# Kernel tuning notes

Hardware: AMD Instinct MI355X
Metric: run time of the kernel (lower is better)

## Reference

```python
import jax, jax.numpy as jnp
import numpy as np

B, T, N, CIN = 64, 24, 256, 1  # batch, n_his, n stations, in channels
F1, F2, OUTC = 64, 128, 1      # blocks [[64,64],[64,128]], output channels
K = 3                          # conv kernel size


def conv2d_same(x, w):  # x [B,H,W,C], w [K,K,C,O]
    return jax.lax.conv_general_dilated(x, w, (1, 1), 'SAME',
                                        dimension_numbers=('NHWC', 'HWIO', 'NHWC'))


def conv1d_same(x, w):  # x [B,N,C], w [K,C,O]
    return jax.lax.conv_general_dilated(x, w, (1,), 'SAME',
                                        dimension_numbers=('NWC', 'WIO', 'NWC'))


def hard_sigmoid(x):  # keras ConvLSTM default recurrent_activation
    return jnp.clip(x * 0.2 + 0.5, 0.0, 1.0)


def l2_normalize_23(x):  # tf.nn.l2_normalize over axes [2,3]
    sq = jnp.sum(x * x, axis=(2, 3), keepdims=True)
    return x * jax.lax.rsqrt(jnp.maximum(sq, 1e-12))


def convlstm1d(x_seq, kx, kh, b, return_sequences):
    # x_seq [B,T,N,C]; kx [K,C,4F]; kh [K,F,4F]; b [4F]
    Bs, Ts, Ns, Cs = x_seq.shape
    F = kh.shape[1]
    # input convolutions are time-independent: do them all at once
    xg = conv1d_same(x_seq.reshape(Bs * Ts, Ns, Cs), kx).reshape(Bs, Ts, Ns, 4 * F) + b
    xg = jnp.moveaxis(xg, 1, 0)  # [T,B,N,4F]
    h0 = jnp.zeros((Bs, Ns, F), x_seq.dtype)
    c0 = jnp.zeros((Bs, Ns, F), x_seq.dtype)

    def step(carry, xt):
        h, c = carry
        g = xt + conv1d_same(h, kh)                 # [B,N,4F]
        gi, gf, gc, go = jnp.split(g, 4, axis=-1)
        i = hard_sigmoid(gi)
        f = hard_sigmoid(gf)
        o = hard_sigmoid(go)
        c = f * c + i * jnp.tanh(gc)
        h = o * jnp.tanh(c)
        return (h, c), (h if return_sequences else jnp.zeros((), x_seq.dtype))

    (hT, _), hs = jax.lax.scan(step, (h0, c0), xg)
    if return_sequences:
        return jnp.moveaxis(hs, 0, 1)  # [B,T,N,F]
    return hT                          # [B,N,F]


def setup_inputs() -> dict:
    key = jax.random.key(0)
    ks = jax.random.split(key, 14)
    s = 0.1
    return {
        'x': jax.random.normal(ks[0], (B, T, N, CIN), jnp.float32),
        'conv1_w': jax.random.normal(ks[1], (K, K, CIN, F1), jnp.float32) * s,
        'conv1_b': jnp.zeros((F1,), jnp.float32),
        'conv2_w': jax.random.normal(ks[2], (K, K, F1, F1), jnp.float32) * s,
        'conv2_b': jnp.zeros((F1,), jnp.float32),
        'kx1': jax.random.normal(ks[3], (K, F1, 4 * F1), jnp.float32) * s,
        'kh1': jax.random.normal(ks[4], (K, F1, 4 * F1), jnp.float32) * s,
        'b1': jnp.zeros((4 * F1,), jnp.float32),
        'kx2': jax.random.normal(ks[5], (K, F1, 4 * F2), jnp.float32) * s,
        'kh2': jax.random.normal(ks[6], (K, F2, 4 * F2), jnp.float32) * s,
        'b2': jnp.zeros((4 * F2,), jnp.float32),
        'fc_w': jax.random.normal(ks[7], (F2, OUTC), jnp.float32) * s,
        'fc_b': jnp.zeros((OUTC,), jnp.float32),
    }


def reference(x, conv1_w, conv1_b, conv2_w, conv2_b, kx1, kh1, b1,
              kx2, kh2, b2, fc_w, fc_b):
    # spatial conv stack (Conv2D 3x3 same, linear activation)
    h = conv2d_same(x, conv1_w) + conv1_b
    h = conv2d_same(h, conv2_w) + conv2_b
    # dropout = identity at inference; norm == 'L2'
    h = l2_normalize_23(h)
    # stacked ConvLSTM1D: return_sequences=True then False
    h = convlstm1d(h, kx1, kh1, b1, True)    # [B,T,N,F1]
    h = convlstm1d(h, kx2, kh2, b2, False)   # [B,N,F2]
    h = h[:, None]                            # reshape (-1, 1, N, F2)
    h = l2_normalize_23(h)
    # FullyConLayer: 1x1 FC over channels -> outc
    y = jnp.einsum('bunc,co->buno', h, fc_w) + fc_b
    return y.reshape(-1, 1, N, OUTC)
```

## Files before the change

### kernel.cpp

```cpp
#include <hip/hip_runtime.h>
#include <hip/hip_bf16.h>

using bf16 = __hip_bfloat16;
typedef unsigned short u16;
typedef unsigned int u32;
typedef __attribute__((ext_vector_type(8))) short short8;
typedef __attribute__((ext_vector_type(4))) float floatx4;

#define DEVI __device__ __forceinline__

constexpr int B = 64, T = 24, N = 256, F1 = 64, F2 = 128;

DEVI float b2f(bf16 v) { return __bfloat162float(v); }
DEVI float b2fu(u16 u) { return __uint_as_float(((u32)u) << 16); }
DEVI u16 f2b(float f) {
    u32 u = __float_as_uint(f);
    u32 r = (u + 0x7FFF + ((u >> 16) & 1)) >> 16;
    return (u16)r;
}
DEVI float hsig(float x) { x = x * 0.2f + 0.5f; return fminf(fmaxf(x, 0.f), 1.f); }

#if __has_builtin(__builtin_amdgcn_global_load_lds)
#define ASYNC16(gsrc, ldst)                                                            \
    __builtin_amdgcn_global_load_lds((const __attribute__((address_space(1))) u32*)(gsrc), \
                                     (__attribute__((address_space(3))) u32*)(ldst), 16, 0, 0)
#define HAVE_ASYNC 1
#else
#define HAVE_ASYNC 0
#endif

DEVI float read_in(const void* p, long i, int isbf) {
    return isbf ? b2f(((const bf16*)p)[i]) : ((const float*)p)[i];
}

__global__ void init_flag(int* flag) { *flag = 1; }
__global__ void detect_scan(const u16* __restrict__ xu, int* __restrict__ flag) {
    int i0 = blockIdx.x * 2048 + threadIdx.x;
    int hit = 0;
    for (int i = i0; i < (blockIdx.x + 1) * 2048; i += 256)
        if (((xu[i] >> 7) & 0xFF) == 0xFF) hit = 1;
    if (hit) *flag = 0;
}

struct CvtDesc { const void* src; float* dst; int n; };
struct CvtPack { CvtDesc d[8]; };
__global__ void cvt_pack(CvtPack p, const int* __restrict__ flag) {
    CvtDesc c = p.d[blockIdx.x];
    int isbf = *flag;
    for (int i = threadIdx.x; i < c.n; i += 256)
        c.dst[i] = c.src ? read_in(c.src, i, isbf) : 0.f;
}

__global__ void repack_w(const void* __restrict__ kxr, const void* __restrict__ khr,
                         u16* __restrict__ Wt, int CIN, int F, const int* __restrict__ flag) {
    int NG = 4 * F, CH = CIN + F, K = 3 * CH;
    int idx = blockIdx.x * 256 + threadIdx.x;
    if (idx >= NG * K) return;
    int g = idx / K, k = idx - g * K;
    int kn = k / CH, c = k - kn * CH;
    int isbf = *flag;
    float v = (c < CIN) ? read_in(kxr, (long)(kn * CIN + c) * NG + g, isbf)
                        : read_in(khr, (long)(kn * F + (c - CIN)) * NG + g, isbf);
    Wt[(long)g * K + k] = f2b(v);
}

__global__ void repack_w2(const void* __restrict__ w2r, u16* __restrict__ w2b,
                          const int* __restrict__ flag) {
    int idx = blockIdx.x * 256 + threadIdx.x;
    if (idx >= 64 * 576) return;
    int f = idx / 576, k = idx - f * 576;
    int kt = k / 192, rem = k - kt * 192, kn = rem >> 6, c = rem & 63;
    float v = read_in(w2r, (long)((kt * 3 + kn) * 64 + c) * 64 + f, *flag);
    w2b[(long)f * 576 + k] = f2b(v);
}

__global__ __launch_bounds__(256)
void conv1_all(const void* __restrict__ xraw, const float* __restrict__ w1c,
               const float* __restrict__ b1v, u16* __restrict__ c1all,
               const int* __restrict__ flag) {
    __shared__ float sxw[3 * 260];
    int s = blockIdx.x, b = blockIdx.y, tid = threadIdx.x;
    int tt = s - 1;
    u16* dst = c1all + ((long)s * B + b) * N * 64;
    if (tt < 0 || tt >= T) {
        for (int i = tid; i < N * 64 / 4; i += 256) *(uint2*)&dst[i * 4] = uint2{0, 0};
        return;
    }
    int isbf = *flag;
    for (int i = tid; i < 3 * 258; i += 256) {
        int r = i / 258, cc = i - r * 258;
        int ttt = tt - 1 + r, nn = cc - 1;
        float v = 0.f;
        if (ttt >= 0 && ttt < T && nn >= 0 && nn < N)
            v = read_in(xraw, (long)(b * T + ttt) * N + nn, isbf);
        sxw[r * 260 + cc] = v;
    }
    __syncthreads();
    int c = tid & 63, ngq = tid >> 6;
    float w[9];
#pragma unroll
    for (int j = 0; j < 9; j++) w[j] = w1c[j * 64 + c];
    float bias = b1v[c];
    for (int j = 0; j < 64; j++) {
        int n = ngq * 64 + j;
        float v = bias;
#pragma unroll
        for (int dt = 0; dt < 3; dt++)
#pragma unroll
            for (int dn = 0; dn < 3; dn++)
                v += sxw[dt * 260 + n + dn] * w[dt * 3 + dn];
        dst[n * 64 + c] = f2b(v);
    }
}

__global__ __launch_bounds__(256)
void conv_mfma(const u16* __restrict__ c1all, const u16* __restrict__ w2b,
               const float* __restrict__ b2v, u16* __restrict__ xs24,
               float* __restrict__ ssq) {
    constexpr int CP1 = 72;
    __shared__ __align__(16) u16 win1[3 * 66 * CP1];
    __shared__ __align__(16) u16 bch[2 * 2048];
    __shared__ float red[256];

    int tid = threadIdx.x;
    int bb = blockIdx.y, n0 = blockIdx.x * 64, t = blockIdx.z;
    int w = tid >> 6, l15 = tid & 15, q = (tid >> 4) & 3;

    for (int i = tid; i < 3 * 66 * 8; i += 256) {
        int u = i & 7, rr = i >> 3;
        int kt = rr / 66, r1 = rr - kt * 66;
        int nn = n0 - 1 + r1;
        uint4 v{0, 0, 0, 0};
        if (nn >= 0 && nn < N)
            v = *(const uint4*)&c1all[((((long)(t + kt)) * B + bb) * N + nn) * 64 + u * 8];
        *(uint4*)&win1[(kt * 66 + r1) * CP1 + u * 8] = v;
    }

    auto stage = [&](int kk, int bufi) {
        int g = tid >> 2, u = tid & 3;
        int k = kk * 32 + ((u ^ (g & 3)) << 3);
#if HAVE_ASYNC
        ASYNC16(w2b + (long)g * 576 + k, &bch[bufi * 2048 + tid * 8]);
#else
        uint4 v = *(const uint4*)(w2b + (long)g * 576 + k);
        *(uint4*)&bch[bufi * 2048 + tid * 8] = v;
#endif
    };
    stage(0, 0);
    __syncthreads();

    floatx4 acc[4] = {};
    for (int kk = 0; kk < 18; ++kk) {
        int cur = kk & 1;
        if (kk + 1 < 18) stage(kk + 1, 1 - cur);
        int kbase = kk * 32;
        int kt = kbase / 192, rem = kbase - kt * 192, kn = rem >> 6, c0 = rem & 63;
        int gcol = w * 16 + l15;
        short8 bf = *(const short8*)&bch[cur * 2048 + gcol * 32 + ((q ^ (gcol & 3)) << 3)];
#pragma unroll
        for (int mi = 0; mi < 4; mi++) {
            short8 af = *(const short8*)&win1[(kt * 66 + mi * 16 + l15 + kn) * CP1 + c0 + q * 8];
            acc[mi] = __builtin_amdgcn_mfma_f32_16x16x32_bf16(af, bf, acc[mi], 0, 0, 0);
        }
        __syncthreads();
    }

    u16* xslice = xs24 + (long)t * B * N * 64;
    int f = w * 16 + l15;
    float bias2 = b2v[f];
    float lsum = 0.f;
#pragma unroll
    for (int mi = 0; mi < 4; mi++)
#pragma unroll
        for (int r = 0; r < 4; r++) {
            int n = n0 + mi * 16 + q * 4 + r;
            float v = acc[mi][r] + bias2;
            lsum += v * v;
            xslice[((long)bb * N + n) * 64 + f] = f2b(v);
        }
    red[tid] = lsum; __syncthreads();
    for (int k = 128; k > 0; k >>= 1) {
        if (tid < k) red[tid] += red[tid + k];
        __syncthreads();
    }
    if (tid == 0) atomicAdd(&ssq[bb * T + t], red[0]);
}

template<int CIN, int F, int FL>
__global__ __launch_bounds__(512, 4)
void lstm_mfma(const u16* __restrict__ xin, const u16* __restrict__ hprev,
               u16* __restrict__ hnext, float* __restrict__ cst,
               const u16* __restrict__ Wt, const float* __restrict__ bias,
               const float* __restrict__ ssqp, int t) {
    constexpr int CH = CIN + F;
    constexpr int CHP = CH + 8;
    constexpr int K = 3 * CH;
    constexpr int NK = K / 32;
    constexpr int NGL = 4 * FL;
    constexpr int NGP = NGL + 4;
    constexpr int NI = NGL / 128;
    constexpr int BCH = NGL * 32;
    constexpr int GLD_USH = 32 * NGP * 2;
    constexpr int UNION_USH = (2 * BCH > GLD_USH) ? 2 * BCH : GLD_USH;
    constexpr int LOGFL = (FL == 64) ? 6 : 5;

    __shared__ __align__(16) u16 win[66 * CHP];
    __shared__ __align__(16) u16 ubuf[UNION_USH];
    u16* bch = ubuf;
    float* Gld = (float*)ubuf;

    int tid = threadIdx.x;
    int bb = blockIdx.y, n0 = blockIdx.x * 64, z = blockIdx.z;
    int w = tid >> 6, l15 = tid & 15, q = (tid >> 4) & 3;

    float scale = 1.f;
    if (ssqp) scale = rsqrtf(fmaxf(ssqp[bb * T + t], 1e-12f));

    constexpr int GRP = CH / 4;
    for (int i = tid; i < 66 * GRP; i += 512) {
        int row = i / GRP, g4 = (i - row * GRP) * 4;
        int n = n0 + row - 1;
        uint2 v{};
        if (n >= 0 && n < N) {
            if (g4 < CIN) {
                v = *(const uint2*)&xin[((long)bb * N + n) * CIN + g4];
                if (ssqp) {
                    u16 e0 = f2b(b2fu((u16)(v.x & 0xFFFF)) * scale);
                    u16 e1 = f2b(b2fu((u16)(v.x >> 16)) * scale);
                    u16 e2 = f2b(b2fu((u16)(v.y & 0xFFFF)) * scale);
                    u16 e3 = f2b(b2fu((u16)(v.y >> 16)) * scale);
                    v.x = (u32)e0 | ((u32)e1 << 16);
                    v.y = (u32)e2 | ((u32)e3 << 16);
                }
            } else if (t > 0) {
                v = *(const uint2*)&hprev[((long)bb * N + n) * F + (g4 - CIN)];
            }
        }
        *(uint2*)&win[row * CHP + g4] = v;
    }

    auto stage = [&](int kk, int bufi) {
#pragma unroll
        for (int it = 0; it < NGL / 128; ++it) {
            int P = it * 512 + tid;
            int r = P >> 2, u = P & 3;
            int gt = r >> LOGFL, fl = r & (FL - 1);
            long g = (long)gt * F + z * FL + fl;
            int k = kk * 32 + ((u ^ (r & 3)) << 3);
#if HAVE_ASYNC
            ASYNC16(Wt + g * K + k, &bch[bufi * BCH + P * 8]);
#else
            uint4 v = *(const uint4*)(Wt + g * K + k);
            *(uint4*)&bch[bufi * BCH + P * 8] = v;
#endif
        }
    };
    stage(0, 0);
    __syncthreads();

    floatx4 acc[4][NI] = {};
    for (int kk = 0; kk < NK; ++kk) {
        int cur = kk & 1;
        if (kk + 1 < NK) stage(kk + 1, 1 - cur);
        int kbase = kk * 32;
        int kn = kbase / CH, c0 = kbase - kn * CH;
        short8 af[4];
#pragma unroll
        for (int mi = 0; mi < 4; mi++)
            af[mi] = *(const short8*)&win[(mi * 16 + l15 + kn) * CHP + c0 + q * 8];
#pragma unroll
        for (int ni = 0; ni < NI; ni++) {
            int r = w * (NI * 16) + ni * 16 + l15;
            short8 bf = *(const short8*)&bch[cur * BCH + r * 32 + ((q ^ (r & 3)) << 3)];
#pragma unroll
            for (int mi = 0; mi < 4; mi++)
                acc[mi][ni] = __builtin_amdgcn_mfma_f32_16x16x32_bf16(af[mi], bf, acc[mi][ni], 0, 0, 0);
        }
        __syncthreads();
    }

    for (int h = 0; h < 2; ++h) {
#pragma unroll
        for (int mi2 = 0; mi2 < 2; ++mi2) {
            int mi = h * 2 + mi2;
#pragma unroll
            for (int ni = 0; ni < NI; ni++)
#pragma unroll
                for (int r = 0; r < 4; r++)
                    Gld[(mi2 * 16 + q * 4 + r) * NGP + w * (NI * 16) + ni * 16 + l15] = acc[mi][ni][r];
        }
        __syncthreads();
        for (int i = tid; i < 32 * FL; i += 512) {
            int m = i >> LOGFL, fl = i & (FL - 1);
            int fz = z * FL + fl;
            float gi = Gld[m * NGP + fl]          + bias[fz];
            float gf = Gld[m * NGP + FL + fl]     + bias[F + fz];
            float gc = Gld[m * NGP + 2 * FL + fl] + bias[2 * F + fz];
            float go = Gld[m * NGP + 3 * FL + fl] + bias[3 * F + fz];
            int n = n0 + h * 32 + m;
            long ci = ((long)bb * N + n) * F + fz;
            float cp = (t > 0) ? cst[ci] : 0.f;
            float iv = hsig(gi), fv = hsig(gf), ov = hsig(go);
            float cn = fv * cp + iv * tanhf(gc);
            cst[ci] = cn;
            hnext[ci] = f2b(ov * tanhf(cn));
        }
        __syncthreads();
    }
}

__global__ void final_kernel(const u16* __restrict__ hT, const float* __restrict__ fcw,
                             const float* __restrict__ fcb, void* __restrict__ out,
                             const int* __restrict__ flag) {
    __shared__ float red[256];
    int b = blockIdx.x, tid = threadIdx.x;
    const u16* hb = hT + (long)b * N * 128;
    float s = 0.f;
    for (int i = tid; i < N * 128; i += 256) { float v = b2fu(hb[i]); s += v * v; }
    red[tid] = s; __syncthreads();
    for (int k = 128; k > 0; k >>= 1) {
        if (tid < k) red[tid] += red[tid + k];
        __syncthreads();
    }
    float scale = rsqrtf(fmaxf(red[0], 1e-12f));
    int n = tid;
    float acc = fcb[0];
    for (int c = 0; c < 128; c++) acc += b2fu(hb[n * 128 + c]) * scale * fcw[c];
    if (*flag) ((bf16*)out)[b * N + n] = __float2bfloat16(acc);
    else       ((float*)out)[b * N + n] = acc;
}

extern "C" void kernel_launch(void* const* d_in, const int* in_sizes, int n_in,
                              void* d_out, int out_size, void* d_ws, size_t ws_size,
                              hipStream_t stream) {
    float* ws = (float*)d_ws;
    u16* xs24   = (u16*)ws;
    u16* c1all  = (u16*)(ws + 12582912);
    u16* h1A    = (u16*)(ws + 26214400);
    u16* h1B    = (u16*)(ws + 26738688);
    u16* h2A    = (u16*)(ws + 27262976);
    u16* h2B    = (u16*)(ws + 28311552);
    float* c1   = ws + 29360128;
    float* c2   = ws + 30408704;
    u16* Wt1    = (u16*)(ws + 32505856);
    u16* Wt2    = (u16*)(ws + 32555008);
    u16* w2b    = (u16*)(ws + 32702464);
    float* w1c  = ws + 32720896;
    float* bb1  = ws + 32721472;
    float* bb2  = ws + 32721536;
    float* bg1  = ws + 32721600;
    float* bg2  = ws + 32721856;
    float* fcwf = ws + 32722368;
    float* fcbf = ws + 32722496;
    float* ssq  = ws + 32722497;
    int*   flag = (int*)(ws + 32724033);

    init_flag<<<1, 1, 0, stream>>>(flag);
    detect_scan<<<32, 256, 0, stream>>>((const u16*)d_in[0], flag);

    CvtPack pk;
    pk.d[0] = {d_in[1],  w1c,  576};
    pk.d[1] = {d_in[2],  bb1,  64};
    pk.d[2] = {d_in[4],  bb2,  64};
    pk.d[3] = {d_in[7],  bg1,  256};
    pk.d[4] = {d_in[10], bg2,  512};
    pk.d[5] = {d_in[11], fcwf, 128};
    pk.d[6] = {d_in[12], fcbf, 1};
    pk.d[7] = {nullptr,  ssq,  B * T};
    cvt_pack<<<8, 256, 0, stream>>>(pk, flag);

    repack_w<<<(256 * 384 + 255) / 256, 256, 0, stream>>>(d_in[5], d_in[6], Wt1, 64, 64, flag);
    repack_w<<<(512 * 576 + 255) / 256, 256, 0, stream>>>(d_in[8], d_in[9], Wt2, 64, 128, flag);
    repack_w2<<<(64 * 576 + 255) / 256, 256, 0, stream>>>(d_in[3], w2b, flag);

    conv1_all<<<dim3(26, B), 256, 0, stream>>>(d_in[0], w1c, bb1, c1all, flag);
    conv_mfma<<<dim3(4, B, 24), 256, 0, stream>>>(c1all, w2b, bb2, xs24, ssq);

    for (int t = 0; t < T; t++) {
        const u16* h1p = (t & 1) ? h1A : h1B;
        u16* h1n = (t & 1) ? h1B : h1A;
        lstm_mfma<64, 64, 32><<<dim3(4, B, 2), 512, 0, stream>>>(
            xs24 + (long)t * B * N * 64, h1p, h1n, c1, Wt1, bg1, ssq, t);
        const u16* h2p = (t & 1) ? h2A : h2B;
        u16* h2n = (t & 1) ? h2B : h2A;
        lstm_mfma<64, 128, 64><<<dim3(4, B, 2), 512, 0, stream>>>(
            h1n, h2p, h2n, c2, Wt2, bg2, nullptr, t);
    }
    final_kernel<<<B, 256, 0, stream>>>(h2B, fcwf, fcbf, d_out, flag);
}
```

Baseline: 970.2 us.

## Load MFMA B-operand weights directly from global into registers, drop LDS staging

Both the conv and LSTM MFMA kernels stop staging weight tiles through double-buffered shared memory with async global-to-LDS loads. Each lane now reads its own B fragment straight from global memory into registers, prefetching one k-step ahead. This removes the per-iteration __syncthreads and shrinks shared memory, since the LSTM kernel can union the window with the gate buffer, which may raise occupancy. The cost is uncoalesced 16-byte global loads per lane that rely on L1/L2 caching of weights shared across blocks.

```diff
diff --git a/kernel.cpp b/kernel.cpp
--- a/kernel.cpp
+++ b/kernel.cpp
@@ -19,15 +19,6 @@
     return (u16)r;
 }
 DEVI float hsig(float x) { x = x * 0.2f + 0.5f; return fminf(fmaxf(x, 0.f), 1.f); }
-
-#if __has_builtin(__builtin_amdgcn_global_load_lds)
-#define ASYNC16(gsrc, ldst)                                                            \
-    __builtin_amdgcn_global_load_lds((const __attribute__((address_space(1))) u32*)(gsrc), \
-                                     (__attribute__((address_space(3))) u32*)(ldst), 16, 0, 0)
-#define HAVE_ASYNC 1
-#else
-#define HAVE_ASYNC 0
-#endif
 
 DEVI float read_in(const void* p, long i, int isbf) {
     return isbf ? b2f(((const bf16*)p)[i]) : ((const float*)p)[i];
@@ -119,7 +110,6 @@
                float* __restrict__ ssq) {
     constexpr int CP1 = 72;
     __shared__ __align__(16) u16 win1[3 * 66 * CP1];
-    __shared__ __align__(16) u16 bch[2 * 2048];
     __shared__ float red[256];
 
     int tid = threadIdx.x;
@@ -135,38 +125,28 @@
             v = *(const uint4*)&c1all[((((long)(t + kt)) * B + bb) * N + nn) * 64 + u * 8];
         *(uint4*)&win1[(kt * 66 + r1) * CP1 + u * 8] = v;
     }
-
-    auto stage = [&](int kk, int bufi) {
-        int g = tid >> 2, u = tid & 3;
-        int k = kk * 32 + ((u ^ (g & 3)) << 3);
-#if HAVE_ASYNC
-        ASYNC16(w2b + (long)g * 576 + k, &bch[bufi * 2048 + tid * 8]);
-#else
-        uint4 v = *(const uint4*)(w2b + (long)g * 576 + k);
-        *(uint4*)&bch[bufi * 2048 + tid * 8] = v;
-#endif
-    };
-    stage(0, 0);
     __syncthreads();
 
+    int gcol = w * 16 + l15;
+    const u16* brow = w2b + (long)gcol * 576 + q * 8;
+    uint4 breg = *(const uint4*)brow;
     floatx4 acc[4] = {};
     for (int kk = 0; kk < 18; ++kk) {
-        int cur = kk & 1;
-        if (kk + 1 < 18) stage(kk + 1, 1 - cur);
+        uint4 bnext;
+        if (kk + 1 < 18) bnext = *(const uint4*)(brow + (kk + 1) * 32);
         int kbase = kk * 32;
         int kt = kbase / 192, rem = kbase - kt * 192, kn = rem >> 6, c0 = rem & 63;
-        int gcol = w * 16 + l15;
-        short8 bf = *(const short8*)&bch[cur * 2048 + gcol * 32 + ((q ^ (gcol & 3)) << 3)];
+        short8 bf = *(short8*)&breg;
 #pragma unroll
         for (int mi = 0; mi < 4; mi++) {
             short8 af = *(const short8*)&win1[(kt * 66 + mi * 16 + l15 + kn) * CP1 + c0 + q * 8];
             acc[mi] = __builtin_amdgcn_mfma_f32_16x16x32_bf16(af, bf, acc[mi], 0, 0, 0);
         }
-        __syncthreads();
+        if (kk + 1 < 18) breg = bnext;
     }
 
     u16* xslice = xs24 + (long)t * B * N * 64;
-    int f = w * 16 + l15;
+    int f = gcol;
     float bias2 = b2v[f];
     float lsum = 0.f;
 #pragma unroll
@@ -199,15 +179,14 @@
     constexpr int NGL = 4 * FL;
     constexpr int NGP = NGL + 4;
     constexpr int NI = NGL / 128;
-    constexpr int BCH = NGL * 32;
+    constexpr int LOGFL = (FL == 64) ? 6 : 5;
+    constexpr int WIN_USH = 66 * CHP;
     constexpr int GLD_USH = 32 * NGP * 2;
-    constexpr int UNION_USH = (2 * BCH > GLD_USH) ? 2 * BCH : GLD_USH;
-    constexpr int LOGFL = (FL == 64) ? 6 : 5;
-
-    __shared__ __align__(16) u16 win[66 * CHP];
-    __shared__ __align__(16) u16 ubuf[UNION_USH];
-    u16* bch = ubuf;
-    float* Gld = (float*)ubuf;
+    constexpr int SM_USH = (WIN_USH > GLD_USH) ? WIN_USH : GLD_USH;
+
+    __shared__ __align__(16) u16 smem[SM_USH];
+    u16* win = smem;
+    float* Gld = (float*)smem;
 
     int tid = threadIdx.x;
     int bb = blockIdx.y, n0 = blockIdx.x * 64, z = blockIdx.z;
@@ -238,30 +217,28 @@
         }
         *(uint2*)&win[row * CHP + g4] = v;
     }
-
-    auto stage = [&](int kk, int bufi) {
-#pragma unroll
-        for (int it = 0; it < NGL / 128; ++it) {
-            int P = it * 512 + tid;
-            int r = P >> 2, u = P & 3;
-            int gt = r >> LOGFL, fl = r & (FL - 1);
-            long g = (long)gt * F + z * FL + fl;
-            int k = kk * 32 + ((u ^ (r & 3)) << 3);
-#if HAVE_ASYNC
-            ASYNC16(Wt + g * K + k, &bch[bufi * BCH + P * 8]);
-#else
-            uint4 v = *(const uint4*)(Wt + g * K + k);
-            *(uint4*)&bch[bufi * BCH + P * 8] = v;
-#endif
-        }
-    };
-    stage(0, 0);
     __syncthreads();
+
+    const u16* brow[NI];
+#pragma unroll
+    for (int ni = 0; ni < NI; ni++) {
+        int r = w * (NI * 16) + ni * 16 + l15;
+        int gt = r >> LOGFL, fl = r & (FL - 1);
+        long g = (long)gt * F + z * FL + fl;
+        brow[ni] = Wt + g * K + q * 8;
+    }
+    uint4 breg[NI];
+#pragma unroll
+    for (int ni = 0; ni < NI; ni++) breg[ni] = *(const uint4*)brow[ni];
 
     floatx4 acc[4][NI] = {};
     for (int kk = 0; kk < NK; ++kk) {
-        int cur = kk & 1;
-        if (kk + 1 < NK) stage(kk + 1, 1 - cur);
+        uint4 bnext[NI];
+        if (kk + 1 < NK) {
+#pragma unroll
+            for (int ni = 0; ni < NI; ni++)
+                bnext[ni] = *(const uint4*)(brow[ni] + (kk + 1) * 32);
+        }
         int kbase = kk * 32;
         int kn = kbase / CH, c0 = kbase - kn * CH;
         short8 af[4];
@@ -270,14 +247,17 @@
             af[mi] = *(const short8*)&win[(mi * 16 + l15 + kn) * CHP + c0 + q * 8];
 #pragma unroll
         for (int ni = 0; ni < NI; ni++) {
-            int r = w * (NI * 16) + ni * 16 + l15;
-            short8 bf = *(const short8*)&bch[cur * BCH + r * 32 + ((q ^ (r & 3)) << 3)];
+            short8 bf = *(short8*)&breg[ni];
 #pragma unroll
             for (int mi = 0; mi < 4; mi++)
                 acc[mi][ni] = __builtin_amdgcn_mfma_f32_16x16x32_bf16(af[mi], bf, acc[mi][ni], 0, 0, 0);
         }
-        __syncthreads();
-    }
+        if (kk + 1 < NK) {
+#pragma unroll
+            for (int ni = 0; ni < NI; ni++) breg[ni] = bnext[ni];
+        }
+    }
+    __syncthreads();
 
     for (int h = 0; h < 2; ++h) {
 #pragma unroll
```

Result: slower. 1.170 ms (+20.6%).

## Run all LSTM1 timesteps in one persistent kernel using halo-overlapped tiles

Applied to the files above, without the earlier changes.

Replaces the 24 per-timestep launches of the first ConvLSTM layer with a single kernel. Each block keeps its weights in registers and its cell state in registers, and recomputes a widening halo (23 extra stations) so it never has to synchronise with neighbouring blocks across timesteps. All h1 outputs are written to a full-sequence buffer that the second-layer launches then read. This removes 24 launches and the global round-trips of h and c, at the cost of redundant halo compute, a large shared-memory footprint and fewer blocks.

```diff
diff --git a/kernel.cpp b/kernel.cpp
--- a/kernel.cpp
+++ b/kernel.cpp
@@ -184,6 +184,109 @@
         __syncthreads();
     }
     if (tid == 0) atomicAdd(&ssq[bb * T + t], red[0]);
+}
+
+__global__ __launch_bounds__(512, 2)
+void lstm1_chain(const u16* __restrict__ xs24, u16* __restrict__ h1all,
+                 const u16* __restrict__ Wt, const float* __restrict__ bias,
+                 const float* __restrict__ ssq) {
+    constexpr int CHP = 136;
+    constexpr int NGP = 260;
+    __shared__ __align__(16) u16 win[114 * CHP];
+    __shared__ __align__(16) float Gld[112 * NGP];
+
+    int tid = threadIdx.x;
+    int bb = blockIdx.y, n0 = blockIdx.x * 64;
+    int lo = n0 - 23; if (lo < 0) lo = 0;
+    int w = tid >> 6, l15 = tid & 15, q = (tid >> 4) & 3;
+
+    uint4 breg[2][12];
+#pragma unroll
+    for (int ni = 0; ni < 2; ni++) {
+        int g = (2 * w + ni) * 16 + l15;
+#pragma unroll
+        for (int kk = 0; kk < 12; kk++)
+            breg[ni][kk] = *(const uint4*)&Wt[(long)g * 384 + kk * 32 + q * 8];
+    }
+
+    float bi[2], bf_[2], bc[2], bo[2];
+    (void)bi; (void)bf_; (void)bc; (void)bo;
+
+    for (int i = tid; i < 114 * CHP / 4; i += 512) *(uint2*)&win[i * 4] = uint2{0, 0};
+    __syncthreads();
+
+    auto stage_x = [&](int t) {
+        float scale = rsqrtf(fmaxf(ssq[bb * T + t], 1e-12f));
+        const u16* xsl = xs24 + (long)t * B * N * 64;
+        for (int i = tid; i < 114 * 16; i += 512) {
+            int r = i >> 4, gi = i & 15;
+            int n = lo - 1 + r;
+            uint2 v{};
+            if (n >= 0 && n < N) {
+                v = *(const uint2*)&xsl[((long)bb * N + n) * 64 + gi * 4];
+                u16 e0 = f2b(b2fu((u16)(v.x & 0xFFFF)) * scale);
+                u16 e1 = f2b(b2fu((u16)(v.x >> 16)) * scale);
+                u16 e2 = f2b(b2fu((u16)(v.y & 0xFFFF)) * scale);
+                u16 e3 = f2b(b2fu((u16)(v.y >> 16)) * scale);
+                v.x = (u32)e0 | ((u32)e1 << 16);
+                v.y = (u32)e2 | ((u32)e3 << 16);
+            }
+            *(uint2*)&win[r * CHP + gi * 4] = v;
+        }
+    };
+    stage_x(0);
+    __syncthreads();
+
+    float cst[14];
+#pragma unroll
+    for (int j = 0; j < 14; j++) cst[j] = 0.f;
+
+    for (int t = 0; t < T; ++t) {
+        floatx4 acc[7][2] = {};
+        for (int kk = 0; kk < 12; ++kk) {
+            int kn = kk >> 2, c0 = (kk & 3) * 32;
+#pragma unroll
+            for (int mi = 0; mi < 7; mi++) {
+                short8 af = *(const short8*)&win[(mi * 16 + l15 + kn) * CHP + c0 + q * 8];
+#pragma unroll
+                for (int ni = 0; ni < 2; ni++)
+                    acc[mi][ni] = __builtin_amdgcn_mfma_f32_16x16x32_bf16(
+                        af, *(short8*)&breg[ni][kk], acc[mi][ni], 0, 0, 0);
+            }
+        }
+#pragma unroll
+        for (int mi = 0; mi < 7; mi++)
+#pragma unroll
+            for (int ni = 0; ni < 2; ni++) {
+                int g = (2 * w + ni) * 16 + l15;
+#pragma unroll
+                for (int r = 0; r < 4; r++)
+                    Gld[(mi * 16 + q * 4 + r) * NGP + g] = acc[mi][ni][r];
+            }
+        __syncthreads();
+
+#pragma unroll
+        for (int j = 0; j < 14; j++) {
+            int p = tid + j * 512;
+            int m = p >> 6, f = p & 63;
+            float gi = Gld[m * NGP + f]        + bias[f];
+            float gf = Gld[m * NGP + 64 + f]   + bias[64 + f];
+            float gc = Gld[m * NGP + 128 + f]  + bias[128 + f];
+            float go = Gld[m * NGP + 192 + f]  + bias[192 + f];
+            float iv = hsig(gi), fv = hsig(gf), ov = hsig(go);
+            float cn = fv * cst[j] + iv * tanhf(gc);
+            cst[j] = cn;
+            int n = lo + m;
+            if (n < N) {
+                u16 hb = f2b(ov * tanhf(cn));
+                win[(m + 1) * CHP + 64 + f] = hb;
+                if ((unsigned)(n - n0) < 64u)
+                    h1all[((long)t * B + bb) * N * 64 + n * 64 + f] = hb;
+            }
+        }
+        if (t + 1 < T) stage_x(t + 1);
+        __syncthreads();
+    }
 }
 
 template<int CIN, int F, int FL>
@@ -336,24 +439,22 @@
     float* ws = (float*)d_ws;
     u16* xs24   = (u16*)ws;
     u16* c1all  = (u16*)(ws + 12582912);
-    u16* h1A    = (u16*)(ws + 26214400);
-    u16* h1B    = (u16*)(ws + 26738688);
-    u16* h2A    = (u16*)(ws + 27262976);
-    u16* h2B    = (u16*)(ws + 28311552);
-    float* c1   = ws + 29360128;
-    float* c2   = ws + 30408704;
-    u16* Wt1    = (u16*)(ws + 32505856);
-    u16* Wt2    = (u16*)(ws + 32555008);
-    u16* w2b    = (u16*)(ws + 32702464);
-    float* w1c  = ws + 32720896;
-    float* bb1  = ws + 32721472;
-    float* bb2  = ws + 32721536;
-    float* bg1  = ws + 32721600;
-    float* bg2  = ws + 32721856;
-    float* fcwf = ws + 32722368;
-    float* fcbf = ws + 32722496;
-    float* ssq  = ws + 32722497;
-    int*   flag = (int*)(ws + 32724033);
+    u16* h1all  = (u16*)(ws + 26214400);
+    u16* h2A    = (u16*)(ws + 38797312);
+    u16* h2B    = (u16*)(ws + 39845888);
+    float* c2   = ws + 40894464;
+    u16* Wt1    = (u16*)(ws + 42991616);
+    u16* Wt2    = (u16*)(ws + 43040768);
+    u16* w2b    = (u16*)(ws + 43188224);
+    float* w1c  = ws + 43206656;
+    float* bb1  = ws + 43207232;
+    float* bb2  = ws + 43207296;
+    float* bg1  = ws + 43207360;
+    float* bg2  = ws + 43207616;
+    float* fcwf = ws + 43208128;
+    float* fcbf = ws + 43208256;
+    float* ssq  = ws + 43208257;
+    int*   flag = (int*)(ws + 43209793);
 
     init_flag<<<1, 1, 0, stream>>>(flag);
     detect_scan<<<32, 256, 0, stream>>>((const u16*)d_in[0], flag);
@@ -376,15 +477,13 @@
     conv1_all<<<dim3(26, B), 256, 0, stream>>>(d_in[0], w1c, bb1, c1all, flag);
     conv_mfma<<<dim3(4, B, 24), 256, 0, stream>>>(c1all, w2b, bb2, xs24, ssq);
 
+    lstm1_chain<<<dim3(4, B), 512, 0, stream>>>(xs24, h1all, Wt1, bg1, ssq);
+
     for (int t = 0; t < T; t++) {
-        const u16* h1p = (t & 1) ? h1A : h1B;
-        u16* h1n = (t & 1) ? h1B : h1A;
-        lstm_mfma<64, 64, 32><<<dim3(4, B, 2), 512, 0, stream>>>(
-            xs24 + (long)t * B * N * 64, h1p, h1n, c1, Wt1, bg1, ssq, t);
         const u16* h2p = (t & 1) ? h2A : h2B;
         u16* h2n = (t & 1) ? h2B : h2A;
         lstm_mfma<64, 128, 64><<<dim3(4, B, 2), 512, 0, stream>>>(
-            h1n, h2p, h2n, c2, Wt2, bg2, nullptr, t);
+            h1all + (long)t * B * N * 64, h2p, h2n, c2, Wt2, bg2, nullptr, t);
     }
     final_kernel<<<B, 256, 0, stream>>>(h2B, fcwf, fcbf, d_out, flag);
 }
```

Measured after the change: 879.2 us. -9.4%, faster.
